# Optimization experiments

Hardware: AMD Instinct MI355X
Metric: run time of the kernel (lower is better)

## Reference

```python
import jax, jax.numpy as jnp
import numpy as np

B, S, D = 16, 2048, 64
K, M = 8, 2048

def setup_inputs() -> dict:
    key = jax.random.key(0)
    kx, kc = jax.random.split(key)
    x = jax.random.normal(kx, (B, S, D), dtype=jnp.float32)
    # nn.init.uniform_(weight, -1/M, 1/M)
    codebooks = jax.random.uniform(kc, (K, M, D), dtype=jnp.float32,
                                   minval=-1.0 / M, maxval=1.0 / M)
    return {"x": x, "codebooks": codebooks}

def reference(x, codebooks):
    """Residual VQ: sequentially quantize residual against K codebooks.

    x: (B,S,D) float32; codebooks: (K,M,D) float32.
    Returns (quantized (B,S,D), indices (K,B,S) int32).
    Uses squared-distance expansion ||r||^2 - 2 r.c + ||c||^2 (argmin-equivalent
    to torch.norm) to avoid materializing the (B,S,M,D) difference tensor.
    """
    def step(residual, cb):  # residual: (B,S,D), cb: (M,D)
        r2 = jnp.sum(residual * residual, axis=-1, keepdims=True)   # (B,S,1)
        c2 = jnp.sum(cb * cb, axis=-1)                              # (M,)
        cross = jnp.einsum('bsd,md->bsm', residual, cb)             # (B,S,M)
        d2 = r2 - 2.0 * cross + c2                                  # (B,S,M)
        idx = jnp.argmin(d2, axis=-1)                               # (B,S)
        q = cb[idx]                                                 # (B,S,D) gather
        return residual - q, idx

    residual, indices = jax.lax.scan(step, x, codebooks)
    quantized = x - residual
    return quantized, indices
```

## Files before the change

kernel.cpp:

```cpp
#include <hip/hip_runtime.h>


#define BB 16
#define SS 2048
#define DD 64
#define KK 8
#define MM 2048
#define NPTS (BB * SS)
#define QSIZE (NPTS * DD)
#define NCHUNK 8
#define WPB 8
#define PPB 512
#define MCHUNK (MM / NCHUNK)

__global__ __launch_bounds__(256) void rvq_prep(const float* __restrict__ cb,
                                                float* __restrict__ c2,
                                                unsigned long long* __restrict__ keys) {
#pragma clang fp contract(off)
    int tid = blockIdx.x * 256 + threadIdx.x;
    const float* row = cb + (size_t)tid * DD;
    float r[8];
#pragma unroll
    for (int j = 0; j < 8; ++j) { float v = row[j]; r[j] = v * v; }
#pragma unroll
    for (int i = 8; i < DD; i += 8) {
#pragma unroll
        for (int j = 0; j < 8; ++j) { float v = row[i + j]; float t = v * v; r[j] += t; }
    }
    c2[tid] = ((r[0] + r[1]) + (r[2] + r[3])) + ((r[4] + r[5]) + (r[6] + r[7]));
    keys[tid] = ~0ULL;
    keys[tid + KK * MM] = ~0ULL;
}

#define R2K(A, B, C, E) \
    "v_pk_mul_f32 v[92:93], v[" A "], v[" A "]\n\t" \
    "v_pk_add_f32 v[80:81], v[80:81], v[92:93]\n\t" \
    "v_pk_mul_f32 v[92:93], v[" B "], v[" B "]\n\t" \
    "v_pk_add_f32 v[82:83], v[82:83], v[92:93]\n\t" \
    "v_pk_mul_f32 v[92:93], v[" C "], v[" C "]\n\t" \
    "v_pk_add_f32 v[84:85], v[84:85], v[92:93]\n\t" \
    "v_pk_mul_f32 v[92:93], v[" E "], v[" E "]\n\t" \
    "v_pk_add_f32 v[86:87], v[86:87], v[92:93]\n\t"

#define GRP(SA, SB, VA, VB) \
    "v_pk_mul_f32 v[84:85], s[" SA "], v[" VA "]\n\t" \
    "v_pk_mul_f32 v[86:87], s[" SB "], v[" VB "]\n\t" \
    "v_pk_add_f32 v[80:81], v[80:81], v[84:85]\n\t" \
    "v_pk_add_f32 v[82:83], v[82:83], v[86:87]\n\t"

__global__ __launch_bounds__(512, 4) void rvq_main(const float* __restrict__ res_in,
                                                   const float* __restrict__ cbk,
                                                   const float* __restrict__ c2k,
                                                   unsigned long long* __restrict__ keys) {
#pragma clang fp contract(off)
    const int tid = threadIdx.x;
    const int lane = tid & 63;
    const int wv = __builtin_amdgcn_readfirstlane(tid >> 6);
    const int ch = blockIdx.x & (NCHUNK - 1);
    const int bp = blockIdx.x >> 3;
    const int point = bp * PPB + wv * 64 + lane;

    const int m0 = ch * MCHUNK;
    const float* cbw = cbk + (size_t)m0 * DD;
    const float* c2w = c2k + m0;
    const unsigned long long ra = (unsigned long long)(res_in + (size_t)point * DD);

    float best;
    int bidx;
    asm volatile(
        "global_load_dwordx4 v[16:19], %[ra], off\n\t"
        "global_load_dwordx4 v[20:23], %[ra], off offset:16\n\t"
        "global_load_dwordx4 v[24:27], %[ra], off offset:32\n\t"
        "global_load_dwordx4 v[28:31], %[ra], off offset:48\n\t"
        "global_load_dwordx4 v[32:35], %[ra], off offset:64\n\t"
        "global_load_dwordx4 v[36:39], %[ra], off offset:80\n\t"
        "global_load_dwordx4 v[40:43], %[ra], off offset:96\n\t"
        "global_load_dwordx4 v[44:47], %[ra], off offset:112\n\t"
        "global_load_dwordx4 v[48:51], %[ra], off offset:128\n\t"
        "global_load_dwordx4 v[52:55], %[ra], off offset:144\n\t"
        "global_load_dwordx4 v[56:59], %[ra], off offset:160\n\t"
        "global_load_dwordx4 v[60:63], %[ra], off offset:176\n\t"
        "global_load_dwordx4 v[64:67], %[ra], off offset:192\n\t"
        "global_load_dwordx4 v[68:71], %[ra], off offset:208\n\t"
        "global_load_dwordx4 v[72:75], %[ra], off offset:224\n\t"
        "global_load_dwordx4 v[76:79], %[ra], off offset:240\n\t"
        "s_waitcnt vmcnt(0)\n\t"
        "v_pk_mul_f32 v[80:81], v[16:17], v[16:17]\n\t"
        "v_pk_mul_f32 v[82:83], v[18:19], v[18:19]\n\t"
        "v_pk_mul_f32 v[84:85], v[20:21], v[20:21]\n\t"
        "v_pk_mul_f32 v[86:87], v[22:23], v[22:23]\n\t"
        R2K("24:25", "26:27", "28:29", "30:31")
        R2K("32:33", "34:35", "36:37", "38:39")
        R2K("40:41", "42:43", "44:45", "46:47")
        R2K("48:49", "50:51", "52:53", "54:55")
        R2K("56:57", "58:59", "60:61", "62:63")
        R2K("64:65", "66:67", "68:69", "70:71")
        R2K("72:73", "74:75", "76:77", "78:79")
        "v_add_f32 v92, v80, v81\n\t"
        "v_add_f32 v93, v82, v83\n\t"
        "v_add_f32 v92, v92, v93\n\t"
        "v_add_f32 v93, v84, v85\n\t"
        "v_add_f32 v88, v86, v87\n\t"
        "v_add_f32 v93, v93, v88\n\t"
        "v_add_f32 v88, v92, v93\n\t"
        "v_mov_b32 v89, 0x7f800000\n\t"
        "v_mov_b32 v90, 0\n\t"
        "s_mov_b32 s29, 0\n\t"
        "Lrvq_%=:\n\t"
        "s_and_b32 s30, s29, 0x7ff\n\t"
        "s_cmp_lg_u32 s30, 0\n\t"
        "s_cbranch_scc1 Lnb_%=\n\t"
        "s_barrier\n\t"
        "Lnb_%=:\n\t"
        "s_load_dwordx16 s[32:47], %[cb], s29\n\t"
        "s_add_u32 s30, s29, 64\n\t"
        "s_load_dwordx16 s[48:63], %[cb], s30\n\t"
        "s_add_u32 s30, s29, 128\n\t"
        "s_load_dwordx16 s[64:79], %[cb], s30\n\t"
        "s_add_u32 s30, s29, 192\n\t"
        "s_load_dwordx16 s[80:95], %[cb], s30\n\t"
        "s_lshr_b32 s31, s29, 6\n\t"
        "s_load_dword s28, %[c2], s31\n\t"
        "s_lshr_b32 s30, s29, 8\n\t"
        "s_add_u32 s30, s30, %[m0]\n\t"
        "v_mov_b32 v91, s30\n\t"
        "s_waitcnt lgkmcnt(0)\n\t"
        "v_pk_mul_f32 v[80:81], s[44:45], v[28:29]\n\t"
        "v_pk_mul_f32 v[82:83], s[46:47], v[30:31]\n\t"
        GRP("40:41", "42:43", "24:25", "26:27")
        GRP("36:37", "38:39", "20:21", "22:23")
        GRP("32:33", "34:35", "16:17", "18:19")
        GRP("60:61", "62:63", "44:45", "46:47")
        GRP("56:57", "58:59", "40:41", "42:43")
        GRP("52:53", "54:55", "36:37", "38:39")
        GRP("48:49", "50:51", "32:33", "34:35")
        GRP("76:77", "78:79", "60:61", "62:63")
        GRP("72:73", "74:75", "56:57", "58:59")
        GRP("68:69", "70:71", "52:53", "54:55")
        GRP("64:65", "66:67", "48:49", "50:51")
        GRP("92:93", "94:95", "76:77", "78:79")
        GRP("88:89", "90:91", "72:73", "74:75")
        GRP("84:85", "86:87", "68:69", "70:71")
        GRP("80:81", "82:83", "64:65", "66:67")
        "v_add_f32 v92, v80, v81\n\t"
        "v_add_f32 v93, v82, v83\n\t"
        "v_add_f32 v92, v92, v93\n\t"
        "v_fma_f32 v92, v92, -2.0, v88\n\t"
        "v_add_f32 v92, s28, v92\n\t"
        "v_cmp_lt_f32 vcc, v92, v89\n\t"
        "v_cndmask_b32 v89, v89, v92, vcc\n\t"
        "v_cndmask_b32 v90, v90, v91, vcc\n\t"
        "s_add_u32 s29, s29, 256\n\t"
        "s_cmp_lg_u32 s29, 0x10000\n\t"
        "s_cbranch_scc1 Lrvq_%=\n\t"
        "v_mov_b32 %[ob], v89\n\t"
        "v_mov_b32 %[oi], v90\n\t"
        : [ob] "=v"(best), [oi] "=v"(bidx)
        : [ra] "v"(ra), [cb] "s"(cbw), [c2] "s"(c2w), [m0] "s"(m0)
        : "vcc", "scc",
          "v16","v17","v18","v19","v20","v21","v22","v23","v24","v25","v26","v27",
          "v28","v29","v30","v31","v32","v33","v34","v35","v36","v37","v38","v39",
          "v40","v41","v42","v43","v44","v45","v46","v47","v48","v49","v50","v51",
          "v52","v53","v54","v55","v56","v57","v58","v59","v60","v61","v62","v63",
          "v64","v65","v66","v67","v68","v69","v70","v71","v72","v73","v74","v75",
          "v76","v77","v78","v79","v80","v81","v82","v83","v84","v85","v86","v87",
          "v88","v89","v90","v91","v92","v93",
          "s28","s29","s30","s31","s32","s33","s34","s35","s36","s37","s38","s39",
          "s40","s41","s42","s43","s44","s45","s46","s47","s48","s49","s50","s51",
          "s52","s53","s54","s55","s56","s57","s58","s59","s60","s61","s62","s63",
          "s64","s65","s66","s67","s68","s69","s70","s71","s72","s73","s74","s75",
          "s76","s77","s78","s79","s80","s81","s82","s83","s84","s85","s86","s87",
          "s88","s89","s90","s91","s92","s93","s94","s95");

    unsigned long long key =
        ((unsigned long long)__float_as_uint(best) << 32) | (unsigned int)bidx;
    atomicMin(&keys[point], key);
}

__global__ __launch_bounds__(256) void rvq_update(const float* __restrict__ res_in,
                                                  float* __restrict__ res_out,
                                                  const float* __restrict__ x,
                                                  const float* __restrict__ cbk,
                                                  unsigned long long* __restrict__ keys,
                                                  float* __restrict__ idx_out,
                                                  int last) {
#pragma clang fp contract(off)
    __shared__ unsigned long long sk[4];
    const int tid = threadIdx.x;
    const int e = blockIdx.x * 256 + tid;
    const int p0 = blockIdx.x * 4;
    if (tid < 4) {
        unsigned long long k = keys[p0 + tid];
        sk[tid] = k;
        keys[p0 + tid] = ~0ULL;
        idx_out[p0 + tid] = (float)(unsigned int)k;
    }
    __syncthreads();
    const int pi = tid >> 6;
    const int d = tid & 63;
    const int m = (int)(unsigned int)sk[pi];
    const float r = res_in[e] - cbk[(size_t)m * DD + d];
    if (last) res_out[e] = x[e] - r;
    else      res_out[e] = r;
}

extern "C" void kernel_launch(void* const* d_in, const int* in_sizes, int n_in,
                              void* d_out, int out_size, void* d_ws, size_t ws_size,
                              hipStream_t stream) {
    const float* x  = (const float*)d_in[0];
    const float* cb = (const float*)d_in[1];

    float* out = (float*)d_out;
    float* quant = out;
    float* idx_out = out + QSIZE;

    float* c2   = (float*)d_ws;
    float* res1 = c2 + (size_t)KK * MM;
    unsigned long long* keys =
        (unsigned long long*)(res1 + (size_t)QSIZE);
    float* R[2] = { quant, res1 };

    rvq_prep<<<(KK * MM) / 256, 256, 0, stream>>>(cb, c2, keys);

    for (int k = 0; k < KK; ++k) {
        const float* rin = (k == 0) ? x : R[(k - 1) & 1];
        const int last = (k == KK - 1);
        float* rout = last ? quant : R[k & 1];
        rvq_main<<<(NPTS / PPB) * NCHUNK, PPB, 0, stream>>>(
            rin,
            cb + (size_t)k * MM * DD,
            c2 + (size_t)k * MM,
            keys);
        rvq_update<<<QSIZE / 256, 256, 0, stream>>>(
            rin, rout, x,
            cb + (size_t)k * MM * DD,
            keys,
            idx_out + (size_t)k * NPTS,
            last);
    }
}
```

Measured before the change: 1.350 ms.

## Split codebook dims between scalar loads and LDS, software-pipeline the row loop

Each block stages the upper 32 dims of its codebook chunk in LDS. The inner loop then takes half of each codeword from scalar memory loads and half from broadcast ds_read_b128, and double-buffers the scalar registers so loads for the next row are issued before the current row's dot product. This is meant to cut scalar-cache load bandwidth per row and hide load latency. In exchange it uses more VGPRs (up to v127), 32KB of LDS per block and an up-front staging pass, which may lower occupancy under launch_bounds(512,4).

```diff
diff --git a/kernel.cpp b/kernel.cpp
--- a/kernel.cpp
+++ b/kernel.cpp
@@ -48,6 +48,78 @@
     "v_pk_add_f32 v[80:81], v[80:81], v[84:85]\n\t" \
     "v_pk_add_f32 v[82:83], v[82:83], v[86:87]\n\t"
 
+#define GRPL(CA, CB, VA, VB) \
+    "v_pk_mul_f32 v[84:85], v[" CA "], v[" VA "]\n\t" \
+    "v_pk_mul_f32 v[86:87], v[" CB "], v[" VB "]\n\t" \
+    "v_pk_add_f32 v[80:81], v[80:81], v[84:85]\n\t" \
+    "v_pk_add_f32 v[82:83], v[82:83], v[86:87]\n\t"
+
+#define SMEMLD(BA, BB, C2D) \
+    "s_min_u32 s30, s29, 0xff00\n\t" \
+    "s_load_dwordx16 s[" BA "], %[cb], s30\n\t" \
+    "s_add_u32 s25, s30, 64\n\t" \
+    "s_load_dwordx16 s[" BB "], %[cb], s25\n\t" \
+    "s_lshr_b32 s25, s30, 6\n\t" \
+    "s_load_dword " C2D ", %[c2], s25\n\t" \
+    "s_add_u32 s29, s29, 256\n\t"
+
+#define DSLD \
+    "ds_read_b128 v[96:99],   v94\n\t" \
+    "ds_read_b128 v[100:103], v94 offset:16\n\t" \
+    "ds_read_b128 v[104:107], v94 offset:32\n\t" \
+    "ds_read_b128 v[108:111], v94 offset:48\n\t" \
+    "ds_read_b128 v[112:115], v94 offset:64\n\t" \
+    "ds_read_b128 v[116:119], v94 offset:80\n\t" \
+    "ds_read_b128 v[120:123], v94 offset:96\n\t" \
+    "ds_read_b128 v[124:127], v94 offset:112\n\t" \
+    "v_add_u32 v94, 0x80, v94\n\t" \
+    "v_min_u32 v94, v95, v94\n\t"
+
+#define EINL \
+    GRPL("108:109","110:111","60:61","62:63") \
+    GRPL("104:105","106:107","56:57","58:59") \
+    GRPL("100:101","102:103","52:53","54:55") \
+    GRPL("96:97","98:99","48:49","50:51") \
+    GRPL("124:125","126:127","76:77","78:79") \
+    GRPL("120:121","122:123","72:73","74:75") \
+    GRPL("116:117","118:119","68:69","70:71") \
+    GRPL("112:113","114:115","64:65","66:67")
+
+#define EINP \
+    "v_pk_mul_f32 v[80:81], s[44:45], v[28:29]\n\t" \
+    "v_pk_mul_f32 v[82:83], s[46:47], v[30:31]\n\t" \
+    GRP("40:41","42:43","24:25","26:27") \
+    GRP("36:37","38:39","20:21","22:23") \
+    GRP("32:33","34:35","16:17","18:19") \
+    GRP("60:61","62:63","44:45","46:47") \
+    GRP("56:57","58:59","40:41","42:43") \
+    GRP("52:53","54:55","36:37","38:39") \
+    GRP("48:49","50:51","32:33","34:35") \
+    EINL
+
+#define EINQ \
+    "v_pk_mul_f32 v[80:81], s[76:77], v[28:29]\n\t" \
+    "v_pk_mul_f32 v[82:83], s[78:79], v[30:31]\n\t" \
+    GRP("72:73","74:75","24:25","26:27") \
+    GRP("68:69","70:71","20:21","22:23") \
+    GRP("64:65","66:67","16:17","18:19") \
+    GRP("92:93","94:95","44:45","46:47") \
+    GRP("88:89","90:91","40:41","42:43") \
+    GRP("84:85","86:87","36:37","38:39") \
+    GRP("80:81","82:83","32:33","34:35") \
+    EINL
+
+#define FINX(C2S) \
+    "v_add_f32 v92, v80, v81\n\t" \
+    "v_add_f32 v93, v82, v83\n\t" \
+    "v_add_f32 v92, v92, v93\n\t" \
+    "v_fma_f32 v92, v92, -2.0, v88\n\t" \
+    "v_add_f32 v92, " C2S ", v92\n\t" \
+    "v_cmp_lt_f32 vcc, v92, v89\n\t" \
+    "v_cndmask_b32 v89, v89, v92, vcc\n\t" \
+    "v_cndmask_b32 v90, v90, v91, vcc\n\t" \
+    "v_add_u32 v91, 1, v91\n\t"
+
 __global__ __launch_bounds__(512, 4) void rvq_main(const float* __restrict__ res_in,
                                                    const float* __restrict__ cbk,
                                                    const float* __restrict__ c2k,
@@ -64,6 +136,16 @@
     const float* cbw = cbk + (size_t)m0 * DD;
     const float* c2w = c2k + m0;
     const unsigned long long ra = (unsigned long long)(res_in + (size_t)point * DD);
+
+    __shared__ __align__(16) float lds_cb[MCHUNK * 32];
+    for (int i = tid; i < MCHUNK * 8; i += PPB) {
+        const int row = i >> 3;
+        const int o = (i & 7) << 2;
+        *(float4*)&lds_cb[row * 32 + o] = *(const float4*)(cbw + row * DD + 32 + o);
+    }
+    __syncthreads();
+    const unsigned ldsbase = (unsigned)(unsigned long long)(void*)&lds_cb[0];
+    const unsigned ldsclamp = ldsbase + (MCHUNK - 1) * 128;
 
     float best;
     int bidx;
@@ -105,72 +187,51 @@
         "v_add_f32 v88, v92, v93\n\t"
         "v_mov_b32 v89, 0x7f800000\n\t"
         "v_mov_b32 v90, 0\n\t"
+        "v_mov_b32 v91, %[m0]\n\t"
+        "v_mov_b32 v94, %[lb]\n\t"
+        "v_mov_b32 v95, %[lc]\n\t"
         "s_mov_b32 s29, 0\n\t"
-        "Lrvq_%=:\n\t"
-        "s_and_b32 s30, s29, 0x7ff\n\t"
-        "s_cmp_lg_u32 s30, 0\n\t"
-        "s_cbranch_scc1 Lnb_%=\n\t"
-        "s_barrier\n\t"
-        "Lnb_%=:\n\t"
-        "s_load_dwordx16 s[32:47], %[cb], s29\n\t"
-        "s_add_u32 s30, s29, 64\n\t"
-        "s_load_dwordx16 s[48:63], %[cb], s30\n\t"
-        "s_add_u32 s30, s29, 128\n\t"
-        "s_load_dwordx16 s[64:79], %[cb], s30\n\t"
-        "s_add_u32 s30, s29, 192\n\t"
-        "s_load_dwordx16 s[80:95], %[cb], s30\n\t"
-        "s_lshr_b32 s31, s29, 6\n\t"
-        "s_load_dword s28, %[c2], s31\n\t"
-        "s_lshr_b32 s30, s29, 8\n\t"
-        "s_add_u32 s30, s30, %[m0]\n\t"
-        "v_mov_b32 v91, s30\n\t"
+        SMEMLD("32:47", "48:63", "s26")
+        DSLD
+        "s_mov_b32 s24, 0\n\t"
+        "Ltop_%=:\n\t"
         "s_waitcnt lgkmcnt(0)\n\t"
-        "v_pk_mul_f32 v[80:81], s[44:45], v[28:29]\n\t"
-        "v_pk_mul_f32 v[82:83], s[46:47], v[30:31]\n\t"
-        GRP("40:41", "42:43", "24:25", "26:27")
-        GRP("36:37", "38:39", "20:21", "22:23")
-        GRP("32:33", "34:35", "16:17", "18:19")
-        GRP("60:61", "62:63", "44:45", "46:47")
-        GRP("56:57", "58:59", "40:41", "42:43")
-        GRP("52:53", "54:55", "36:37", "38:39")
-        GRP("48:49", "50:51", "32:33", "34:35")
-        GRP("76:77", "78:79", "60:61", "62:63")
-        GRP("72:73", "74:75", "56:57", "58:59")
-        GRP("68:69", "70:71", "52:53", "54:55")
-        GRP("64:65", "66:67", "48:49", "50:51")
-        GRP("92:93", "94:95", "76:77", "78:79")
-        GRP("88:89", "90:91", "72:73", "74:75")
-        GRP("84:85", "86:87", "68:69", "70:71")
-        GRP("80:81", "82:83", "64:65", "66:67")
-        "v_add_f32 v92, v80, v81\n\t"
-        "v_add_f32 v93, v82, v83\n\t"
-        "v_add_f32 v92, v92, v93\n\t"
-        "v_fma_f32 v92, v92, -2.0, v88\n\t"
-        "v_add_f32 v92, s28, v92\n\t"
-        "v_cmp_lt_f32 vcc, v92, v89\n\t"
-        "v_cndmask_b32 v89, v89, v92, vcc\n\t"
-        "v_cndmask_b32 v90, v90, v91, vcc\n\t"
-        "s_add_u32 s29, s29, 256\n\t"
-        "s_cmp_lg_u32 s29, 0x10000\n\t"
-        "s_cbranch_scc1 Lrvq_%=\n\t"
+        SMEMLD("64:79", "80:95", "s27")
+        EINP
+        DSLD
+        FINX("s26")
+        "s_waitcnt lgkmcnt(0)\n\t"
+        SMEMLD("32:47", "48:63", "s26")
+        EINQ
+        DSLD
+        FINX("s27")
+        "s_add_u32 s24, s24, 1\n\t"
+        "s_cmp_lg_u32 s24, 128\n\t"
+        "s_cbranch_scc1 Ltop_%=\n\t"
+        "s_waitcnt lgkmcnt(0)\n\t"
         "v_mov_b32 %[ob], v89\n\t"
         "v_mov_b32 %[oi], v90\n\t"
         : [ob] "=v"(best), [oi] "=v"(bidx)
-        : [ra] "v"(ra), [cb] "s"(cbw), [c2] "s"(c2w), [m0] "s"(m0)
+        : [ra] "v"(ra), [cb] "s"(cbw), [c2] "s"(c2w), [m0] "s"(m0),
+          [lb] "s"(ldsbase), [lc] "s"(ldsclamp)
         : "vcc", "scc",
+          "s24","s25","s26","s27","s29","s30",
+          "s32","s33","s34","s35","s36","s37","s38","s39",
+          "s40","s41","s42","s43","s44","s45","s46","s47","s48","s49","s50","s51",
+          "s52","s53","s54","s55","s56","s57","s58","s59","s60","s61","s62","s63",
+          "s64","s65","s66","s67","s68","s69","s70","s71","s72","s73","s74","s75",
+          "s76","s77","s78","s79","s80","s81","s82","s83","s84","s85","s86","s87",
+          "s88","s89","s90","s91","s92","s93","s94","s95",
           "v16","v17","v18","v19","v20","v21","v22","v23","v24","v25","v26","v27",
           "v28","v29","v30","v31","v32","v33","v34","v35","v36","v37","v38","v39",
           "v40","v41","v42","v43","v44","v45","v46","v47","v48","v49","v50","v51",
           "v52","v53","v54","v55","v56","v57","v58","v59","v60","v61","v62","v63",
           "v64","v65","v66","v67","v68","v69","v70","v71","v72","v73","v74","v75",
           "v76","v77","v78","v79","v80","v81","v82","v83","v84","v85","v86","v87",
-          "v88","v89","v90","v91","v92","v93",
-          "s28","s29","s30","s31","s32","s33","s34","s35","s36","s37","s38","s39",
-          "s40","s41","s42","s43","s44","s45","s46","s47","s48","s49","s50","s51",
-          "s52","s53","s54","s55","s56","s57","s58","s59","s60","s61","s62","s63",
-          "s64","s65","s66","s67","s68","s69","s70","s71","s72","s73","s74","s75",
-          "s76","s77","s78","s79","s80","s81","s82","s83","s84","s85","s86","s87",
-          "s88","s89","s90","s91","s92","s93","s94","s95");
+          "v88","v89","v90","v91","v92","v93","v94","v95","v96","v97","v98","v99",
+          "v100","v101","v102","v103","v104","v105","v106","v107","v108","v109",
+          "v110","v111","v112","v113","v114","v115","v116","v117","v118","v119",
+          "v120","v121","v122","v123","v124","v125","v126","v127");
 
     unsigned long long key =
         ((unsigned long long)__float_as_uint(best) << 32) | (unsigned int)bidx;
```

New measurement: 1.317 ms. -2.4%, faster.
